# Performance work log

Measured on AMD Instinct MI355X. Metric: run time of the kernel, lower is better.

Reference implementation:

```python
import jax, jax.numpy as jnp
import numpy as np

TOP_K = 2
TEMP = 1.0  # router_temperature
B, L, D, F, DF, DR, DH, E = 32, 256, 256, 8, 64, 256, 512, 8
DIN = D + DF  # expert/router input: concat(hidden, feat_emb)


def setup_inputs() -> dict:
    key = jax.random.key(0)
    ks = jax.random.split(key, 12)
    gn = lambda k, shape, fan: jax.random.normal(k, shape, dtype=jnp.float32) * (fan ** -0.5)
    return {
        "hidden": jax.random.normal(ks[0], (B, L, D), dtype=jnp.float32),
        "feat": jax.random.uniform(ks[1], (B, L, F), dtype=jnp.float32),
        "W_feat": gn(ks[2], (F, DF), F),
        "b_feat": jnp.zeros((DF,), jnp.float32),
        "Wr1": gn(ks[3], (DIN, DR), DIN),
        "br1": jnp.zeros((DR,), jnp.float32),
        "Wr2": gn(ks[4], (DR, E), DR),
        "br2": jnp.zeros((E,), jnp.float32),
        "We1": gn(ks[5], (E, DIN, DH), DIN),
        "be1": jnp.zeros((E, DH), jnp.float32),
        "We2": gn(ks[6], (E, DH, D), DH),
        "be2": jnp.zeros((E, D), jnp.float32),
    }


def reference(hidden, feat, W_feat, b_feat, Wr1, br1, Wr2, br2, We1, be1, We2, be2):
    # feature embedding
    feat_emb = feat @ W_feat + b_feat                       # [B,L,DF]
    x = jnp.concatenate([hidden, feat_emb], axis=-1)        # [B,L,DIN]

    # token-level learned router with temperature + top-k gating
    hr = jax.nn.gelu(x @ Wr1 + br1)                         # [B,L,DR]
    gate_logits = (hr @ Wr2 + br2) / TEMP                   # [B,L,E]
    topv, topi = jax.lax.top_k(gate_logits, TOP_K)          # [B,L,K]
    w = jax.nn.softmax(topv, axis=-1)                       # renormalized over top-k
    gate_weights = (jax.nn.one_hot(topi, E, dtype=w.dtype) * w[..., None]).sum(-2)  # [B,L,E]

    # experts: per-expert 2-layer MLP (dense compute, sparse combine via gates)
    he = jax.nn.gelu(jnp.einsum('bli,eih->bleh', x, We1) + be1)   # [B,L,E,DH]
    eo = jnp.einsum('bleh,eho->bleo', he, We2) + be2              # [B,L,E,D]
    stage_delta = jnp.einsum('ble,bleo->blo', gate_weights, eo)   # next_hidden - hidden

    return stage_delta, gate_weights, gate_logits
```

## Files before the change

### kernel.cpp

```cpp
#include <hip/hip_runtime.h>
#include <hip/hip_bf16.h>

#define N_TOK   8192
#define DMODEL  256
#define NFEAT   8
#define DFEAT   64
#define DIN     320
#define DRTR    256
#define NE      8
#define DH      512
#define TE      32
#define RTB     32
#define FIXCAP  128
#define FIXTHR  2e-3f

#define OUT_GATEW  (N_TOK*DMODEL)
#define OUT_LOGITS (N_TOK*DMODEL + N_TOK*NE)

typedef short v8s __attribute__((ext_vector_type(8)));
typedef float v4f __attribute__((ext_vector_type(4)));

__device__ __forceinline__ unsigned short f2bf(float f){
  unsigned u = __float_as_uint(f);
  return (unsigned short)((u + 0x7FFFu + ((u>>16)&1u)) >> 16);
}
__device__ __forceinline__ float bf2f(unsigned short h){
  return __uint_as_float(((unsigned)h)<<16);
}
__device__ __forceinline__ float gelu_tanh(float v){
  float u = 0.7978845608028654f * (v + 0.044715f * v * v * v);
  float a = fabsf(u);
  float e = __expf(-2.0f * a);
  float t = (1.0f - e) / (1.0f + e);
  t = copysignf(t, u);
  return 0.5f * v * (1.0f + t);
}

__global__ void k_init(int* __restrict__ cnts, int* __restrict__ nfix){
  if (threadIdx.x < NE) cnts[threadIdx.x] = 0;
  if (threadIdx.x == NE) *nfix = 0;
}

__global__ __launch_bounds__(256) void k_prep1(const float* __restrict__ W,
                                               unsigned short* __restrict__ dh,
                                               unsigned short* __restrict__ dl){
  int gid = blockIdx.x*256 + threadIdx.x;
  int l = gid & 63; int w = gid >> 6;
  int nt = w & 31; w >>= 5; int kstep = w % 10; int e = w / 10;
  int n = nt*16 + (l&15);
  int kb = kstep*32 + ((l>>4)<<3);
  const float* src = W + ((size_t)e*DIN + kb)*DH + n;
  unsigned short hs[8], ls[8];
  #pragma unroll
  for (int i=0;i<8;i++){
    float v = src[(size_t)i*DH];
    unsigned short h = f2bf(v);
    hs[i] = h; ls[i] = f2bf(v - bf2f(h));
  }
  size_t off = (size_t)gid*8;
  *(v8s*)(dh+off) = *(v8s*)hs;
  *(v8s*)(dl+off) = *(v8s*)ls;
}

__global__ __launch_bounds__(256) void k_prep2(const float* __restrict__ W,
                                               unsigned short* __restrict__ dh,
                                               unsigned short* __restrict__ dl){
  int gid = blockIdx.x*256 + threadIdx.x;
  int l = gid & 63; int w = gid >> 6;
  int nt = w & 15; w >>= 4; int kstep = w & 15; int e = w >> 4;
  int n = nt*16 + (l&15);
  int kb = kstep*32 + ((l>>4)<<3);
  const float* src = W + ((size_t)e*DH + kb)*DMODEL + n;
  unsigned short hs[8], ls[8];
  #pragma unroll
  for (int i=0;i<8;i++){
    float v = src[(size_t)i*DMODEL];
    unsigned short h = f2bf(v);
    hs[i] = h; ls[i] = f2bf(v - bf2f(h));
  }
  size_t off = (size_t)gid*8;
  *(v8s*)(dh+off) = *(v8s*)hs;
  *(v8s*)(dl+off) = *(v8s*)ls;
}

__global__ __launch_bounds__(256) void k_prepr(const float* __restrict__ W,
                                               unsigned short* __restrict__ dh,
                                               unsigned short* __restrict__ dl){
  int gid = blockIdx.x*256 + threadIdx.x;
  if (gid >= 10240) return;
  int l = gid & 63; int w = gid >> 6;
  int nt = w & 15; int kstep = w >> 4;
  int n = nt*16 + (l&15);
  int kb = kstep*32 + ((l>>4)<<3);
  const float* src = W + (size_t)kb*DRTR + n;
  unsigned short hs[8], ls[8];
  #pragma unroll
  for (int i=0;i<8;i++){
    float v = src[(size_t)i*DRTR];
    unsigned short h = f2bf(v);
    hs[i] = h; ls[i] = f2bf(v - bf2f(h));
  }
  size_t off = (size_t)gid*8;
  *(v8s*)(dh+off) = *(v8s*)hs;
  *(v8s*)(dl+off) = *(v8s*)ls;
}

#define MM6(c0,c1,ah0,ah1,al0,al1,bh,bl) do{ \
  c0 = __builtin_amdgcn_mfma_f32_16x16x32_bf16(ah0, bh, c0, 0,0,0); \
  c1 = __builtin_amdgcn_mfma_f32_16x16x32_bf16(ah1, bh, c1, 0,0,0); \
  c0 = __builtin_amdgcn_mfma_f32_16x16x32_bf16(al0, bh, c0, 0,0,0); \
  c1 = __builtin_amdgcn_mfma_f32_16x16x32_bf16(al1, bh, c1, 0,0,0); \
  c0 = __builtin_amdgcn_mfma_f32_16x16x32_bf16(ah0, bl, c0, 0,0,0); \
  c1 = __builtin_amdgcn_mfma_f32_16x16x32_bf16(ah1, bl, c1, 0,0,0); }while(0)

#define XLOFF  10496
#define HELOFF 16640

__global__ __launch_bounds__(512) void k_rmfma(
    const float* __restrict__ hidden, const float* __restrict__ feat,
    const float* __restrict__ Wf, const float* __restrict__ bfe,
    const unsigned short* __restrict__ Wr1h, const unsigned short* __restrict__ Wr1l,
    const float* __restrict__ br1,
    const float* __restrict__ Wr2, const float* __restrict__ br2,
    float* __restrict__ out,
    int* __restrict__ cnts, unsigned* __restrict__ lists, float* __restrict__ topw,
    int* __restrict__ nfix, int* __restrict__ fixlist)
{
  __shared__ unsigned short sm[21248];
  __shared__ float part_lds[512];
  __shared__ float lg_lds[RTB*NE];
  float* hrf = (float*)sm;
  const int tid = threadIdx.x;
  const int t0 = blockIdx.x * RTB;

  {
    float4 z = make_float4(0.f,0.f,0.f,0.f);
    float4* dst = ((float4*)out) + (size_t)blockIdx.x*2048 + tid;
    #pragma unroll
    for (int r=0;r<4;r++) dst[r*512] = z;
  }
  #pragma unroll
  for (int r=0;r<4;r++){
    int idx = r*512 + tid; int t = idx >> 6, lane = idx & 63;
    float4 h4 = ((const float4*)(hidden + (size_t)(t0+t)*DMODEL))[lane];
    unsigned short h0=f2bf(h4.x),h1=f2bf(h4.y),h2=f2bf(h4.z),h3=f2bf(h4.w);
    unsigned short l0=f2bf(h4.x-bf2f(h0)),l1=f2bf(h4.y-bf2f(h1)),
                   l2=f2bf(h4.z-bf2f(h2)),l3=f2bf(h4.w-bf2f(h3));
    uint2 hp, lp;
    hp.x=(unsigned)h0|((unsigned)h1<<16); hp.y=(unsigned)h2|((unsigned)h3<<16);
    lp.x=(unsigned)l0|((unsigned)l1<<16); lp.y=(unsigned)l2|((unsigned)l3<<16);
    *(uint2*)&sm[t*328 + lane*4]         = hp;
    *(uint2*)&sm[XLOFF + t*328 + lane*4] = lp;
  }
  #pragma unroll
  for (int r=0;r<4;r++){
    int idx = r*512 + tid; int t = idx >> 6, j = idx & 63;
    float acc = bfe[j];
    #pragma unroll
    for (int f=0; f<NFEAT; f++) acc += feat[(size_t)(t0+t)*NFEAT + f] * Wf[f*DFEAT + j];
    unsigned short h = f2bf(acc);
    sm[t*328 + DMODEL + j]         = h;
    sm[XLOFF + t*328 + DMODEL + j] = f2bf(acc - bf2f(h));
  }
  __syncthreads();

  const int wv = tid >> 6;
  const int l  = tid & 63;
  const int lg = l >> 4;
  const int lr = l & 15;

  v4f acc[2][2];
  {
    v4f z = {0.f,0.f,0.f,0.f};
    acc[0][0]=z; acc[0][1]=z; acc[1][0]=z; acc[1][1]=z;
    v8s bh_a[2], bl_a[2], bh_b[2], bl_b[2];
    auto ldBr = [&](int ks, v8s (&bh)[2], v8s (&bl)[2]){
      #pragma unroll
      for (int j=0;j<2;++j){
        size_t boff = ((size_t)(ks*16 + wv*2 + j)*64 + l)*8;
        bh[j] = *(const v8s*)(Wr1h + boff);
        bl[j] = *(const v8s*)(Wr1l + boff);
      }
    };
    ldBr(0, bh_a, bl_a);
    for (int ks=0; ks<10; ks+=2){
      v8s ah0 = *(const v8s*)&sm[( 0+lr)*328 + ks*32 + lg*8];
      v8s ah1 = *(const v8s*)&sm[(16+lr)*328 + ks*32 + lg*8];
      v8s al0 = *(const v8s*)&sm[XLOFF + ( 0+lr)*328 + ks*32 + lg*8];
      v8s al1 = *(const v8s*)&sm[XLOFF + (16+lr)*328 + ks*32 + lg*8];
      ldBr(ks+1, bh_b, bl_b);
      #pragma unroll
      for (int j=0;j<2;++j) MM6(acc[0][j],acc[1][j], ah0,ah1,al0,al1, bh_a[j],bl_a[j]);
      v8s ch0 = *(const v8s*)&sm[( 0+lr)*328 + (ks+1)*32 + lg*8];
      v8s ch1 = *(const v8s*)&sm[(16+lr)*328 + (ks+1)*32 + lg*8];
      v8s cl0 = *(const v8s*)&sm[XLOFF + ( 0+lr)*328 + (ks+1)*32 + lg*8];
      v8s cl1 = *(const v8s*)&sm[XLOFF + (16+lr)*328 + (ks+1)*32 + lg*8];
      if (ks+2<10) ldBr(ks+2, bh_a, bl_a);
      #pragma unroll
      for (int j=0;j<2;++j) MM6(acc[0][j],acc[1][j], ch0,ch1,cl0,cl1, bh_b[j],bl_b[j]);
    }
  }
  __syncthreads();
  #pragma unroll
  for (int j=0;j<2;++j){
    int col = (wv*2+j)*16 + lr;
    float b1 = br1[col];
    #pragma unroll
    for (int m=0;m<2;m++)
      #pragma unroll
      for (int r=0;r<4;r++){
        int row = m*16 + lg*4 + r;
        hrf[row*264 + col] = gelu_tanh(acc[m][j][r] + b1);
      }
  }
  __syncthreads();
  {
    int q = tid >> 8, rr = tid & 255, t = rr >> 3, e = rr & 7;
    float a0=0.f,a1=0.f,a2=0.f,a3=0.f;
    #pragma unroll 4
    for (int k4=0;k4<32;k4++){
      float4 h4 = ((const float4*)hrf)[t*66 + q*32 + k4];
      int row = q*128 + k4*4;
      a0 += h4.x * Wr2[(row+0)*NE + e];
      a1 += h4.y * Wr2[(row+1)*NE + e];
      a2 += h4.z * Wr2[(row+2)*NE + e];
      a3 += h4.w * Wr2[(row+3)*NE + e];
    }
    part_lds[tid] = (a0+a1)+(a2+a3);
  }
  __syncthreads();
  if (tid < RTB*NE){
    int t = tid >> 3, e = tid & 7;
    float lgv = br2[e] + part_lds[tid] + part_lds[tid+256];
    out[OUT_LOGITS + (size_t)(t0+t)*NE + e] = lgv;
    lg_lds[t*NE + e] = lgv;
  }
  __syncthreads();
  if (tid < RTB){
    int t = tid, tok = t0 + t;
    float v1=-3.4e38f, v2=-3.4e38f, v3=-3.4e38f; int i1=-1, i2=-1;
    #pragma unroll
    for (int e=0;e<NE;e++){
      float v = lg_lds[t*NE+e];
      if (v > v1){ v3=v2; v2=v1; i2=i1; v1=v; i1=e; }
      else if (v > v2){ v3=v2; v2=v; i2=e; }
      else if (v > v3){ v3=v; }
    }
    bool defer = false;
    if (v2 - v3 < FIXTHR){
      int fi = atomicAdd(nfix, 1);
      if (fi < FIXCAP){ fixlist[fi] = tok; defer = true; }
    }
    if (!defer){
      float d   = expf(v2 - v1);
      float inv = 1.0f/(1.0f + d);
      float w1 = inv, w2 = d*inv;
      #pragma unroll
      for (int e=0;e<NE;e++){
        float gv = (e==i1) ? w1 : ((e==i2) ? w2 : 0.f);
        out[OUT_GATEW + (size_t)tok*NE + e] = gv;
      }
      int p1 = atomicAdd(&cnts[i1], 1);
      lists[i1*N_TOK + p1] = (unsigned)(tok<<1);
      int p2 = atomicAdd(&cnts[i2], 1);
      lists[i2*N_TOK + p2] = (unsigned)((tok<<1) | 1);
      topw[tok*2]   = w1;
      topw[tok*2+1] = w2;
    }
  }
}

__global__ __launch_bounds__(256) void k_fix(
    const float* __restrict__ hidden, const float* __restrict__ feat,
    const float* __restrict__ Wf, const float* __restrict__ bfe,
    const float* __restrict__ Wr1, const float* __restrict__ br1,
    const float* __restrict__ Wr2, const float* __restrict__ br2,
    float* __restrict__ out, const int* __restrict__ nfix, const int* __restrict__ fixlist)
{
  int nf = *nfix; if (nf > FIXCAP) nf = FIXCAP;
  if ((int)blockIdx.x >= nf) return;
  const int tok = fixlist[blockIdx.x];
  const int tid = threadIdx.x;
  __shared__ float xf[DIN];
  __shared__ float hr[DRTR];
  if (tid < DMODEL) xf[tid] = hidden[(size_t)tok*DMODEL + tid];
  if (tid < DFEAT){
    float acc = bfe[tid];
    #pragma unroll
    for (int f=0; f<NFEAT; f++) acc += feat[(size_t)tok*NFEAT + f] * Wf[f*DFEAT + tid];
    xf[DMODEL + tid] = acc;
  }
  __syncthreads();
  {
    float acc = br1[tid];
    for (int i=0;i<DIN;i++) acc += xf[i] * Wr1[(size_t)i*DRTR + tid];
    hr[tid] = gelu_tanh(acc);
  }
  __syncthreads();
  if (tid < NE){
    float acc = br2[tid];
    for (int i=0;i<DRTR;i++) acc += hr[i] * Wr2[i*NE + tid];
    out[OUT_LOGITS + (size_t)tok*NE + tid] = acc;
  }
}

__global__ void k_gatefix(float* __restrict__ out,
                          int* __restrict__ cnts, unsigned* __restrict__ lists,
                          float* __restrict__ topw,
                          const int* __restrict__ nfix, const int* __restrict__ fixlist)
{
  int nf = *nfix; if (nf > FIXCAP) nf = FIXCAP;
  int i = threadIdx.x;
  if (i >= nf) return;
  int tok = fixlist[i];
  float v1=-3.4e38f, v2=-3.4e38f; int i1=-1, i2=-1;
  #pragma unroll
  for (int e=0;e<NE;e++){
    float v = out[OUT_LOGITS + (size_t)tok*NE + e];
    if (v > v1){ v2=v1; i2=i1; v1=v; i1=e; }
    else if (v > v2){ v2=v; i2=e; }
  }
  float d   = expf(v2 - v1);
  float inv = 1.0f/(1.0f + d);
  float w1 = inv, w2 = d*inv;
  #pragma unroll
  for (int e=0;e<NE;e++){
    float gv = (e==i1) ? w1 : ((e==i2) ? w2 : 0.f);
    out[OUT_GATEW + (size_t)tok*NE + e] = gv;
  }
  int p1 = atomicAdd(&cnts[i1], 1);
  lists[i1*N_TOK + p1] = (unsigned)(tok<<1);
  int p2 = atomicAdd(&cnts[i2], 1);
  lists[i2*N_TOK + p2] = (unsigned)((tok<<1) | 1);
  topw[tok*2]   = w1;
  topw[tok*2+1] = w2;
}

__global__ __launch_bounds__(512) void k_expert(
    const float* __restrict__ hidden, const float* __restrict__ feat,
    const float* __restrict__ Wf, const float* __restrict__ bfe,
    const int* __restrict__ cnts, const unsigned* __restrict__ lists,
    const float* __restrict__ topw,
    const unsigned short* __restrict__ W1h, const unsigned short* __restrict__ W1l,
    const unsigned short* __restrict__ W2h, const unsigned short* __restrict__ W2l,
    const float* __restrict__ be1, const float* __restrict__ be2,
    float* __restrict__ out)
{
  __shared__ unsigned short sm[33280];
  __shared__ int   tok_lds[TE];
  __shared__ float w_lds[TE];

  const int e    = blockIdx.x & 7;
  const int tile = blockIdx.x >> 3;
  const int cnt  = cnts[e];
  const int start = tile * TE;
  if (start >= cnt) return;
  const int ntk = min(TE, cnt - start);
  const int tid = threadIdx.x;

  if (tid < TE){
    if (tid < ntk){
      unsigned ent = lists[e*N_TOK + start + tid];
      int tok = (int)(ent >> 1);
      tok_lds[tid] = tok;
      w_lds[tid]   = topw[tok*2 + (ent & 1)];
    } else { tok_lds[tid] = -1; w_lds[tid] = 0.f; }
  }
  __syncthreads();
  #pragma unroll
  for (int r=0;r<4;r++){
    int idx = r*512 + tid; int t = idx >> 6, lane = idx & 63;
    int tok = tok_lds[t];
    float4 h4 = make_float4(0.f,0.f,0.f,0.f);
    if (tok >= 0) h4 = ((const float4*)(hidden + (size_t)tok*DMODEL))[lane];
    unsigned short h0=f2bf(h4.x),h1=f2bf(h4.y),h2=f2bf(h4.z),h3=f2bf(h4.w);
    unsigned short l0=f2bf(h4.x-bf2f(h0)),l1=f2bf(h4.y-bf2f(h1)),
                   l2=f2bf(h4.z-bf2f(h2)),l3=f2bf(h4.w-bf2f(h3));
    uint2 hp, lp;
    hp.x=(unsigned)h0|((unsigned)h1<<16); hp.y=(unsigned)h2|((unsigned)h3<<16);
    lp.x=(unsigned)l0|((unsigned)l1<<16); lp.y=(unsigned)l2|((unsigned)l3<<16);
    *(uint2*)&sm[t*328 + lane*4]         = hp;
    *(uint2*)&sm[XLOFF + t*328 + lane*4] = lp;
  }
  #pragma unroll
  for (int r=0;r<4;r++){
    int idx = r*512 + tid; int t = idx >> 6, j = idx & 63;
    int tok = tok_lds[t];
    float acc = 0.f;
    if (tok >= 0){
      acc = bfe[j];
      #pragma unroll
      for (int f=0; f<NFEAT; f++) acc += feat[(size_t)tok*NFEAT + f] * Wf[f*DFEAT + j];
    }
    unsigned short h = f2bf(acc);
    sm[t*328 + DMODEL + j]         = h;
    sm[XLOFF + t*328 + DMODEL + j] = f2bf(acc - bf2f(h));
  }
  __syncthreads();

  const int wv = tid >> 6;
  const int l  = tid & 63;
  const int lg = l >> 4;
  const int lr = l & 15;

  v4f acc1[2][4];
  {
    v4f z = {0.f,0.f,0.f,0.f};
    #pragma unroll
    for (int m=0;m<2;m++)
      #pragma unroll
      for (int j=0;j<4;j++) acc1[m][j] = z;
    const unsigned short* p1h = W1h + (size_t)e*163840;
    const unsigned short* p1l = W1l + (size_t)e*163840;
    auto ldB1 = [&](int ks, int jh, v8s (&bh)[2], v8s (&bl)[2]){
      #pragma unroll
      for (int j=0;j<2;++j){
        size_t boff = ((size_t)(ks*32 + wv*4 + jh*2 + j)*64 + l)*8;
        bh[j] = *(const v8s*)(p1h + boff);
        bl[j] = *(const v8s*)(p1l + boff);
      }
    };
    v8s bh_a[2], bl_a[2], bh_b[2], bl_b[2];
    ldB1(0,0,bh_a,bl_a);
    for (int ks=0; ks<10; ++ks){
      v8s ah0 = *(const v8s*)&sm[( 0+lr)*328 + ks*32 + lg*8];
      v8s ah1 = *(const v8s*)&sm[(16+lr)*328 + ks*32 + lg*8];
      v8s al0 = *(const v8s*)&sm[XLOFF + ( 0+lr)*328 + ks*32 + lg*8];
      v8s al1 = *(const v8s*)&sm[XLOFF + (16+lr)*328 + ks*32 + lg*8];
      ldB1(ks,1,bh_b,bl_b);
      #pragma unroll
      for (int j=0;j<2;++j) MM6(acc1[0][j],acc1[1][j], ah0,ah1,al0,al1, bh_a[j],bl_a[j]);
      if (ks<9) ldB1(ks+1,0,bh_a,bl_a);
      #pragma unroll
      for (int j=0;j<2;++j) MM6(acc1[0][2+j],acc1[1][2+j], ah0,ah1,al0,al1, bh_b[j],bl_b[j]);
    }
  }
  __syncthreads();
  #pragma unroll
  for (int j=0;j<4;++j){
    int col = (wv*4+j)*16 + lr;
    float b1 = be1[e*DH + col];
    #pragma unroll
    for (int m=0;m<2;m++)
      #pragma unroll
      for (int r=0;r<4;r++){
        float v = gelu_tanh(acc1[m][j][r] + b1);
        int row = m*16 + lg*4 + r;
        unsigned short h = f2bf(v);
        sm[row*520 + col]          = h;
        sm[HELOFF + row*520 + col] = f2bf(v - bf2f(h));
      }
  }
  __syncthreads();
  v4f acc2[2][2];
  {
    v4f z = {0.f,0.f,0.f,0.f};
    acc2[0][0]=z; acc2[0][1]=z; acc2[1][0]=z; acc2[1][1]=z;
    const unsigned short* p2h = W2h + (size_t)e*131072;
    const unsigned short* p2l = W2l + (size_t)e*131072;
    auto ldB2 = [&](int ks, v8s (&bh)[2], v8s (&bl)[2]){
      #pragma unroll
      for (int j=0;j<2;++j){
        size_t boff = ((size_t)(ks*16 + wv*2 + j)*64 + l)*8;
        bh[j] = *(const v8s*)(p2h + boff);
        bl[j] = *(const v8s*)(p2l + boff);
      }
    };
    v8s bh_a[2], bl_a[2], bh_b[2], bl_b[2];
    ldB2(0,bh_a,bl_a);
    for (int ks=0; ks<16; ks+=2){
      v8s ah0 = *(const v8s*)&sm[( 0+lr)*520 + ks*32 + lg*8];
      v8s ah1 = *(const v8s*)&sm[(16+lr)*520 + ks*32 + lg*8];
      v8s al0 = *(const v8s*)&sm[HELOFF + ( 0+lr)*520 + ks*32 + lg*8];
      v8s al1 = *(const v8s*)&sm[HELOFF + (16+lr)*520 + ks*32 + lg*8];
      ldB2(ks+1, bh_b, bl_b);
      #pragma unroll
      for (int j=0;j<2;++j) MM6(acc2[0][j],acc2[1][j], ah0,ah1,al0,al1, bh_a[j],bl_a[j]);
      v8s ch0 = *(const v8s*)&sm[( 0+lr)*520 + (ks+1)*32 + lg*8];
      v8s ch1 = *(const v8s*)&sm[(16+lr)*520 + (ks+1)*32 + lg*8];
      v8s cl0 = *(const v8s*)&sm[HELOFF + ( 0+lr)*520 + (ks+1)*32 + lg*8];
      v8s cl1 = *(const v8s*)&sm[HELOFF + (16+lr)*520 + (ks+1)*32 + lg*8];
      if (ks+2<16) ldB2(ks+2, bh_a, bl_a);
      #pragma unroll
      for (int j=0;j<2;++j) MM6(acc2[0][j],acc2[1][j], ch0,ch1,cl0,cl1, bh_b[j],bl_b[j]);
    }
  }
  #pragma unroll
  for (int j=0;j<2;++j){
    int col = (wv*2+j)*16 + lr;
    float b2 = be2[e*DMODEL + col];
    #pragma unroll
    for (int m=0;m<2;m++)
      #pragma unroll
      for (int r=0;r<4;r++){
        int row = m*16 + lg*4 + r;
        if (row < ntk){
          float w = w_lds[row];
          atomicAdd(out + (size_t)tok_lds[row]*DMODEL + col,
                    w*(acc2[m][j][r] + b2));
        }
      }
  }
}

extern "C" void kernel_launch(void* const* d_in, const int* in_sizes, int n_in,
                              void* d_out, int out_size, void* d_ws, size_t ws_size,
                              hipStream_t stream)
{
  (void)in_sizes; (void)n_in; (void)out_size; (void)ws_size;
  const float* hidden = (const float*)d_in[0];
  const float* feat   = (const float*)d_in[1];
  const float* Wf     = (const float*)d_in[2];
  const float* bfe    = (const float*)d_in[3];
  const float* Wr1    = (const float*)d_in[4];
  const float* br1    = (const float*)d_in[5];
  const float* Wr2    = (const float*)d_in[6];
  const float* br2    = (const float*)d_in[7];
  const float* We1    = (const float*)d_in[8];
  const float* be1    = (const float*)d_in[9];
  const float* We2    = (const float*)d_in[10];
  const float* be2    = (const float*)d_in[11];
  float* out = (float*)d_out;

  char* ws = (char*)d_ws;
  int*      cnts    = (int*)ws;
  int*      nfix    = (int*)(ws + 64);
  int*      fixlist = (int*)(ws + 128);
  unsigned* lists   = (unsigned*)(ws + 1024);
  float*    topw    = (float*)(ws + 263168);
  unsigned short* W1h  = (unsigned short*)(ws + 328704);
  unsigned short* W1l  = (unsigned short*)(ws + 2950144);
  unsigned short* W2h  = (unsigned short*)(ws + 5571584);
  unsigned short* W2l  = (unsigned short*)(ws + 7668736);
  unsigned short* Wr1h = (unsigned short*)(ws + 9765888);
  unsigned short* Wr1l = (unsigned short*)(ws + 9929728);

  hipLaunchKernelGGL(k_init, dim3(1), dim3(64), 0, stream, cnts, nfix);
  hipLaunchKernelGGL(k_prep1, dim3(640), dim3(256), 0, stream, We1, W1h, W1l);
  hipLaunchKernelGGL(k_prep2, dim3(512), dim3(256), 0, stream, We2, W2h, W2l);
  hipLaunchKernelGGL(k_prepr, dim3(40),  dim3(256), 0, stream, Wr1, Wr1h, Wr1l);
  hipLaunchKernelGGL(k_rmfma, dim3(N_TOK/RTB), dim3(512), 0, stream,
                     hidden, feat, Wf, bfe, Wr1h, Wr1l, br1, Wr2, br2,
                     out, cnts, lists, topw, nfix, fixlist);
  hipLaunchKernelGGL(k_fix, dim3(FIXCAP), dim3(256), 0, stream,
                     hidden, feat, Wf, bfe, Wr1, br1, Wr2, br2, out, nfix, fixlist);
  hipLaunchKernelGGL(k_gatefix, dim3(1), dim3(FIXCAP), 0, stream,
                     out, cnts, lists, topw, nfix, fixlist);
  hipLaunchKernelGGL(k_expert, dim3((N_TOK/TE)*NE), dim3(512), 0, stream,
                     hidden, feat, Wf, bfe, cnts, lists, topw,
                     W1h, W1l, W2h, W2l, be1, be2, out);
}
```

Baseline: 293.8 us.

## Double expert token tile to 64 with 1024-thread blocks; merge prep kernels

The expert kernel now processes 64 routed tokens per block with 16 waves instead of 32 tokens with 8 waves. Each wave owns fewer output columns but more row tiles, so every bf16 hi/lo expert weight fragment loaded from global memory is reused across twice as many tokens. The first weight fragments are prefetched before the token gather to hide load latency. Separately, the three weight-split prep kernels and the counter-init kernel are merged into one launch to cut launch overhead. The cost is about 133KB of LDS per block, which limits occupancy to one block per CU, and more padded work on the last partial tile of each expert.

```diff
diff --git a/kernel.cpp b/kernel.cpp
--- a/kernel.cpp
+++ b/kernel.cpp
@@ -9,7 +9,7 @@
 #define DRTR    256
 #define NE      8
 #define DH      512
-#define TE      32
+#define TE      64
 #define RTB     32
 #define FIXCAP  128
 #define FIXTHR  2e-3f
@@ -36,73 +36,71 @@
   return 0.5f * v * (1.0f + t);
 }
 
-__global__ void k_init(int* __restrict__ cnts, int* __restrict__ nfix){
-  if (threadIdx.x < NE) cnts[threadIdx.x] = 0;
-  if (threadIdx.x == NE) *nfix = 0;
-}
-
-__global__ __launch_bounds__(256) void k_prep1(const float* __restrict__ W,
-                                               unsigned short* __restrict__ dh,
-                                               unsigned short* __restrict__ dl){
-  int gid = blockIdx.x*256 + threadIdx.x;
-  int l = gid & 63; int w = gid >> 6;
-  int nt = w & 31; w >>= 5; int kstep = w % 10; int e = w / 10;
-  int n = nt*16 + (l&15);
-  int kb = kstep*32 + ((l>>4)<<3);
-  const float* src = W + ((size_t)e*DIN + kb)*DH + n;
-  unsigned short hs[8], ls[8];
-  #pragma unroll
-  for (int i=0;i<8;i++){
-    float v = src[(size_t)i*DH];
-    unsigned short h = f2bf(v);
-    hs[i] = h; ls[i] = f2bf(v - bf2f(h));
-  }
-  size_t off = (size_t)gid*8;
-  *(v8s*)(dh+off) = *(v8s*)hs;
-  *(v8s*)(dl+off) = *(v8s*)ls;
-}
-
-__global__ __launch_bounds__(256) void k_prep2(const float* __restrict__ W,
-                                               unsigned short* __restrict__ dh,
-                                               unsigned short* __restrict__ dl){
-  int gid = blockIdx.x*256 + threadIdx.x;
-  int l = gid & 63; int w = gid >> 6;
-  int nt = w & 15; w >>= 4; int kstep = w & 15; int e = w >> 4;
-  int n = nt*16 + (l&15);
-  int kb = kstep*32 + ((l>>4)<<3);
-  const float* src = W + ((size_t)e*DH + kb)*DMODEL + n;
-  unsigned short hs[8], ls[8];
-  #pragma unroll
-  for (int i=0;i<8;i++){
-    float v = src[(size_t)i*DMODEL];
-    unsigned short h = f2bf(v);
-    hs[i] = h; ls[i] = f2bf(v - bf2f(h));
-  }
-  size_t off = (size_t)gid*8;
-  *(v8s*)(dh+off) = *(v8s*)hs;
-  *(v8s*)(dl+off) = *(v8s*)ls;
-}
-
-__global__ __launch_bounds__(256) void k_prepr(const float* __restrict__ W,
-                                               unsigned short* __restrict__ dh,
-                                               unsigned short* __restrict__ dl){
-  int gid = blockIdx.x*256 + threadIdx.x;
-  if (gid >= 10240) return;
-  int l = gid & 63; int w = gid >> 6;
-  int nt = w & 15; int kstep = w >> 4;
-  int n = nt*16 + (l&15);
-  int kb = kstep*32 + ((l>>4)<<3);
-  const float* src = W + (size_t)kb*DRTR + n;
-  unsigned short hs[8], ls[8];
-  #pragma unroll
-  for (int i=0;i<8;i++){
-    float v = src[(size_t)i*DRTR];
-    unsigned short h = f2bf(v);
-    hs[i] = h; ls[i] = f2bf(v - bf2f(h));
-  }
-  size_t off = (size_t)gid*8;
-  *(v8s*)(dh+off) = *(v8s*)hs;
-  *(v8s*)(dl+off) = *(v8s*)ls;
+__global__ __launch_bounds__(256) void k_prep(
+    const float* __restrict__ We1, const float* __restrict__ We2,
+    const float* __restrict__ Wr1,
+    unsigned short* __restrict__ W1h, unsigned short* __restrict__ W1l,
+    unsigned short* __restrict__ W2h, unsigned short* __restrict__ W2l,
+    unsigned short* __restrict__ Wr1h, unsigned short* __restrict__ Wr1l,
+    int* __restrict__ cnts, int* __restrict__ nfix)
+{
+  const int b = blockIdx.x;
+  const int tid = threadIdx.x;
+  if (b < 640){
+    int gid = b*256 + tid;
+    int l = gid & 63; int w = gid >> 6;
+    int nt = w & 31; w >>= 5; int kstep = w % 10; int e = w / 10;
+    int n = nt*16 + (l&15);
+    int kb = kstep*32 + ((l>>4)<<3);
+    const float* src = We1 + ((size_t)e*DIN + kb)*DH + n;
+    unsigned short hs[8], ls[8];
+    #pragma unroll
+    for (int i=0;i<8;i++){
+      float v = src[(size_t)i*DH];
+      unsigned short h = f2bf(v);
+      hs[i] = h; ls[i] = f2bf(v - bf2f(h));
+    }
+    size_t off = (size_t)gid*8;
+    *(v8s*)(W1h+off) = *(v8s*)hs;
+    *(v8s*)(W1l+off) = *(v8s*)ls;
+  } else if (b < 1152){
+    int gid = (b-640)*256 + tid;
+    int l = gid & 63; int w = gid >> 6;
+    int nt = w & 15; w >>= 4; int kstep = w & 15; int e = w >> 4;
+    int n = nt*16 + (l&15);
+    int kb = kstep*32 + ((l>>4)<<3);
+    const float* src = We2 + ((size_t)e*DH + kb)*DMODEL + n;
+    unsigned short hs[8], ls[8];
+    #pragma unroll
+    for (int i=0;i<8;i++){
+      float v = src[(size_t)i*DMODEL];
+      unsigned short h = f2bf(v);
+      hs[i] = h; ls[i] = f2bf(v - bf2f(h));
+    }
+    size_t off = (size_t)gid*8;
+    *(v8s*)(W2h+off) = *(v8s*)hs;
+    *(v8s*)(W2l+off) = *(v8s*)ls;
+  } else if (b < 1192){
+    int gid = (b-1152)*256 + tid;
+    int l = gid & 63; int w = gid >> 6;
+    int nt = w & 15; int kstep = w >> 4;
+    int n = nt*16 + (l&15);
+    int kb = kstep*32 + ((l>>4)<<3);
+    const float* src = Wr1 + (size_t)kb*DRTR + n;
+    unsigned short hs[8], ls[8];
+    #pragma unroll
+    for (int i=0;i<8;i++){
+      float v = src[(size_t)i*DRTR];
+      unsigned short h = f2bf(v);
+      hs[i] = h; ls[i] = f2bf(v - bf2f(h));
+    }
+    size_t off = (size_t)gid*8;
+    *(v8s*)(Wr1h+off) = *(v8s*)hs;
+    *(v8s*)(Wr1l+off) = *(v8s*)ls;
+  } else {
+    if (tid < NE) cnts[tid] = 0;
+    if (tid == NE) *nfix = 0;
+  }
 }
 
 #define MM6(c0,c1,ah0,ah1,al0,al1,bh,bl) do{ \
@@ -114,7 +112,6 @@
   c1 = __builtin_amdgcn_mfma_f32_16x16x32_bf16(ah1, bl, c1, 0,0,0); }while(0)
 
 #define XLOFF  10496
-#define HELOFF 16640
 
 __global__ __launch_bounds__(512) void k_rmfma(
     const float* __restrict__ hidden, const float* __restrict__ feat,
@@ -336,7 +333,9 @@
   topw[tok*2+1] = w2;
 }
 
-__global__ __launch_bounds__(512) void k_expert(
+#define XL2   20992
+#define HEL2  33280
+__global__ __launch_bounds__(1024, 4) void k_expert(
     const float* __restrict__ hidden, const float* __restrict__ feat,
     const float* __restrict__ Wf, const float* __restrict__ bfe,
     const int* __restrict__ cnts, const unsigned* __restrict__ lists,
@@ -346,7 +345,7 @@
     const float* __restrict__ be1, const float* __restrict__ be2,
     float* __restrict__ out)
 {
-  __shared__ unsigned short sm[33280];
+  __shared__ unsigned short sm[66560];
   __shared__ int   tok_lds[TE];
   __shared__ float w_lds[TE];
 
@@ -357,6 +356,21 @@
   if (start >= cnt) return;
   const int ntk = min(TE, cnt - start);
   const int tid = threadIdx.x;
+  const int wv = tid >> 6;
+  const int l  = tid & 63;
+  const int lg = l >> 4;
+  const int lr = l & 15;
+
+  const unsigned short* p1h = W1h + (size_t)e*163840;
+  const unsigned short* p1l = W1l + (size_t)e*163840;
+
+  v8s bhA[2], blA[2], bhB[2], blB[2];
+  #pragma unroll
+  for (int j=0;j<2;++j){
+    size_t boff = ((size_t)(wv*2 + j)*64 + l)*8;
+    bhA[j] = *(const v8s*)(p1h + boff);
+    blA[j] = *(const v8s*)(p1l + boff);
+  }
 
   if (tid < TE){
     if (tid < ntk){
@@ -369,7 +383,7 @@
   __syncthreads();
   #pragma unroll
   for (int r=0;r<4;r++){
-    int idx = r*512 + tid; int t = idx >> 6, lane = idx & 63;
+    int idx = r*1024 + tid; int t = idx >> 6, lane = idx & 63;
     int tok = tok_lds[t];
     float4 h4 = make_float4(0.f,0.f,0.f,0.f);
     if (tok >= 0) h4 = ((const float4*)(hidden + (size_t)tok*DMODEL))[lane];
@@ -379,12 +393,12 @@
     uint2 hp, lp;
     hp.x=(unsigned)h0|((unsigned)h1<<16); hp.y=(unsigned)h2|((unsigned)h3<<16);
     lp.x=(unsigned)l0|((unsigned)l1<<16); lp.y=(unsigned)l2|((unsigned)l3<<16);
-    *(uint2*)&sm[t*328 + lane*4]         = hp;
-    *(uint2*)&sm[XLOFF + t*328 + lane*4] = lp;
+    *(uint2*)&sm[t*328 + lane*4]       = hp;
+    *(uint2*)&sm[XL2 + t*328 + lane*4] = lp;
   }
   #pragma unroll
   for (int r=0;r<4;r++){
-    int idx = r*512 + tid; int t = idx >> 6, j = idx & 63;
+    int idx = r*1024 + tid; int t = idx >> 6, j = idx & 63;
     int tok = tok_lds[t];
     float acc = 0.f;
     if (tok >= 0){
@@ -393,111 +407,140 @@
       for (int f=0; f<NFEAT; f++) acc += feat[(size_t)tok*NFEAT + f] * Wf[f*DFEAT + j];
     }
     unsigned short h = f2bf(acc);
-    sm[t*328 + DMODEL + j]         = h;
-    sm[XLOFF + t*328 + DMODEL + j] = f2bf(acc - bf2f(h));
-  }
-  __syncthreads();
-
-  const int wv = tid >> 6;
-  const int l  = tid & 63;
-  const int lg = l >> 4;
-  const int lr = l & 15;
-
-  v4f acc1[2][4];
+    sm[t*328 + DMODEL + j]       = h;
+    sm[XL2 + t*328 + DMODEL + j] = f2bf(acc - bf2f(h));
+  }
+  __syncthreads();
+
+  v4f acc1[4][2];
   {
     v4f z = {0.f,0.f,0.f,0.f};
     #pragma unroll
-    for (int m=0;m<2;m++)
-      #pragma unroll
-      for (int j=0;j<4;j++) acc1[m][j] = z;
-    const unsigned short* p1h = W1h + (size_t)e*163840;
-    const unsigned short* p1l = W1l + (size_t)e*163840;
-    auto ldB1 = [&](int ks, int jh, v8s (&bh)[2], v8s (&bl)[2]){
+    for (int m=0;m<4;m++){ acc1[m][0]=z; acc1[m][1]=z; }
+    for (int ks=0; ks<10; ks+=2){
+      v8s ah[4], al[4];
+      #pragma unroll
+      for (int m=0;m<4;m++){
+        ah[m] = *(const v8s*)&sm[(m*16+lr)*328 + ks*32 + lg*8];
+        al[m] = *(const v8s*)&sm[XL2 + (m*16+lr)*328 + ks*32 + lg*8];
+      }
       #pragma unroll
       for (int j=0;j<2;++j){
-        size_t boff = ((size_t)(ks*32 + wv*4 + jh*2 + j)*64 + l)*8;
-        bh[j] = *(const v8s*)(p1h + boff);
-        bl[j] = *(const v8s*)(p1l + boff);
-      }
-    };
-    v8s bh_a[2], bl_a[2], bh_b[2], bl_b[2];
-    ldB1(0,0,bh_a,bl_a);
-    for (int ks=0; ks<10; ++ks){
-      v8s ah0 = *(const v8s*)&sm[( 0+lr)*328 + ks*32 + lg*8];
-      v8s ah1 = *(const v8s*)&sm[(16+lr)*328 + ks*32 + lg*8];
-      v8s al0 = *(const v8s*)&sm[XLOFF + ( 0+lr)*328 + ks*32 + lg*8];
-      v8s al1 = *(const v8s*)&sm[XLOFF + (16+lr)*328 + ks*32 + lg*8];
-      ldB1(ks,1,bh_b,bl_b);
-      #pragma unroll
-      for (int j=0;j<2;++j) MM6(acc1[0][j],acc1[1][j], ah0,ah1,al0,al1, bh_a[j],bl_a[j]);
-      if (ks<9) ldB1(ks+1,0,bh_a,bl_a);
-      #pragma unroll
-      for (int j=0;j<2;++j) MM6(acc1[0][2+j],acc1[1][2+j], ah0,ah1,al0,al1, bh_b[j],bl_b[j]);
-    }
-  }
-  __syncthreads();
-  #pragma unroll
-  for (int j=0;j<4;++j){
-    int col = (wv*4+j)*16 + lr;
+        size_t boff = ((size_t)((ks+1)*32 + wv*2 + j)*64 + l)*8;
+        bhB[j] = *(const v8s*)(p1h + boff);
+        blB[j] = *(const v8s*)(p1l + boff);
+      }
+      #pragma unroll
+      for (int j=0;j<2;++j){
+        #pragma unroll
+        for (int m=0;m<4;m++) acc1[m][j] = __builtin_amdgcn_mfma_f32_16x16x32_bf16(ah[m], bhA[j], acc1[m][j], 0,0,0);
+        #pragma unroll
+        for (int m=0;m<4;m++) acc1[m][j] = __builtin_amdgcn_mfma_f32_16x16x32_bf16(al[m], bhA[j], acc1[m][j], 0,0,0);
+        #pragma unroll
+        for (int m=0;m<4;m++) acc1[m][j] = __builtin_amdgcn_mfma_f32_16x16x32_bf16(ah[m], blA[j], acc1[m][j], 0,0,0);
+      }
+      #pragma unroll
+      for (int m=0;m<4;m++){
+        ah[m] = *(const v8s*)&sm[(m*16+lr)*328 + (ks+1)*32 + lg*8];
+        al[m] = *(const v8s*)&sm[XL2 + (m*16+lr)*328 + (ks+1)*32 + lg*8];
+      }
+      if (ks+2<10){
+        #pragma unroll
+        for (int j=0;j<2;++j){
+          size_t boff = ((size_t)((ks+2)*32 + wv*2 + j)*64 + l)*8;
+          bhA[j] = *(const v8s*)(p1h + boff);
+          blA[j] = *(const v8s*)(p1l + boff);
+        }
+      }
+      #pragma unroll
+      for (int j=0;j<2;++j){
+        #pragma unroll
+        for (int m=0;m<4;m++) acc1[m][j] = __builtin_amdgcn_mfma_f32_16x16x32_bf16(ah[m], bhB[j], acc1[m][j], 0,0,0);
+        #pragma unroll
+        for (int m=0;m<4;m++) acc1[m][j] = __builtin_amdgcn_mfma_f32_16x16x32_bf16(al[m], bhB[j], acc1[m][j], 0,0,0);
+        #pragma unroll
+        for (int m=0;m<4;m++) acc1[m][j] = __builtin_amdgcn_mfma_f32_16x16x32_bf16(ah[m], blB[j], acc1[m][j], 0,0,0);
+      }
+    }
+  }
+  const unsigned short* p2h = W2h + (size_t)e*131072;
+  const unsigned short* p2l = W2l + (size_t)e*131072;
+  v8s c2hA, c2lA, c2hB, c2lB;
+  {
+    size_t boff = ((size_t)wv*64 + l)*8;
+    c2hA = *(const v8s*)(p2h + boff);
+    c2lA = *(const v8s*)(p2l + boff);
+  }
+  __syncthreads();
+  #pragma unroll
+  for (int j=0;j<2;++j){
+    int col = (wv*2+j)*16 + lr;
     float b1 = be1[e*DH + col];
     #pragma unroll
-    for (int m=0;m<2;m++)
+    for (int m=0;m<4;m++)
       #pragma unroll
       for (int r=0;r<4;r++){
         float v = gelu_tanh(acc1[m][j][r] + b1);
         int row = m*16 + lg*4 + r;
         unsigned short h = f2bf(v);
-        sm[row*520 + col]          = h;
-        sm[HELOFF + row*520 + col] = f2bf(v - bf2f(h));
-      }
-  }
-  __syncthreads();
-  v4f acc2[2][2];
+        sm[row*520 + col]        = h;
+        sm[HEL2 + row*520 + col] = f2bf(v - bf2f(h));
+      }
+  }
+  __syncthreads();
+  v4f acc2[4];
   {
     v4f z = {0.f,0.f,0.f,0.f};
-    acc2[0][0]=z; acc2[0][1]=z; acc2[1][0]=z; acc2[1][1]=z;
-    const unsigned short* p2h = W2h + (size_t)e*131072;
-    const unsigned short* p2l = W2l + (size_t)e*131072;
-    auto ldB2 = [&](int ks, v8s (&bh)[2], v8s (&bl)[2]){
-      #pragma unroll
-      for (int j=0;j<2;++j){
-        size_t boff = ((size_t)(ks*16 + wv*2 + j)*64 + l)*8;
-        bh[j] = *(const v8s*)(p2h + boff);
-        bl[j] = *(const v8s*)(p2l + boff);
-      }
-    };
-    v8s bh_a[2], bl_a[2], bh_b[2], bl_b[2];
-    ldB2(0,bh_a,bl_a);
+    #pragma unroll
+    for (int m=0;m<4;m++) acc2[m] = z;
     for (int ks=0; ks<16; ks+=2){
-      v8s ah0 = *(const v8s*)&sm[( 0+lr)*520 + ks*32 + lg*8];
-      v8s ah1 = *(const v8s*)&sm[(16+lr)*520 + ks*32 + lg*8];
-      v8s al0 = *(const v8s*)&sm[HELOFF + ( 0+lr)*520 + ks*32 + lg*8];
-      v8s al1 = *(const v8s*)&sm[HELOFF + (16+lr)*520 + ks*32 + lg*8];
-      ldB2(ks+1, bh_b, bl_b);
-      #pragma unroll
-      for (int j=0;j<2;++j) MM6(acc2[0][j],acc2[1][j], ah0,ah1,al0,al1, bh_a[j],bl_a[j]);
-      v8s ch0 = *(const v8s*)&sm[( 0+lr)*520 + (ks+1)*32 + lg*8];
-      v8s ch1 = *(const v8s*)&sm[(16+lr)*520 + (ks+1)*32 + lg*8];
-      v8s cl0 = *(const v8s*)&sm[HELOFF + ( 0+lr)*520 + (ks+1)*32 + lg*8];
-      v8s cl1 = *(const v8s*)&sm[HELOFF + (16+lr)*520 + (ks+1)*32 + lg*8];
-      if (ks+2<16) ldB2(ks+2, bh_a, bl_a);
-      #pragma unroll
-      for (int j=0;j<2;++j) MM6(acc2[0][j],acc2[1][j], ch0,ch1,cl0,cl1, bh_b[j],bl_b[j]);
-    }
-  }
-  #pragma unroll
-  for (int j=0;j<2;++j){
-    int col = (wv*2+j)*16 + lr;
+      v8s ah[4], al[4];
+      #pragma unroll
+      for (int m=0;m<4;m++){
+        ah[m] = *(const v8s*)&sm[(m*16+lr)*520 + ks*32 + lg*8];
+        al[m] = *(const v8s*)&sm[HEL2 + (m*16+lr)*520 + ks*32 + lg*8];
+      }
+      {
+        size_t boff = ((size_t)((ks+1)*16 + wv)*64 + l)*8;
+        c2hB = *(const v8s*)(p2h + boff);
+        c2lB = *(const v8s*)(p2l + boff);
+      }
+      #pragma unroll
+      for (int m=0;m<4;m++) acc2[m] = __builtin_amdgcn_mfma_f32_16x16x32_bf16(ah[m], c2hA, acc2[m], 0,0,0);
+      #pragma unroll
+      for (int m=0;m<4;m++) acc2[m] = __builtin_amdgcn_mfma_f32_16x16x32_bf16(al[m], c2hA, acc2[m], 0,0,0);
+      #pragma unroll
+      for (int m=0;m<4;m++) acc2[m] = __builtin_amdgcn_mfma_f32_16x16x32_bf16(ah[m], c2lA, acc2[m], 0,0,0);
+      #pragma unroll
+      for (int m=0;m<4;m++){
+        ah[m] = *(const v8s*)&sm[(m*16+lr)*520 + (ks+1)*32 + lg*8];
+        al[m] = *(const v8s*)&sm[HEL2 + (m*16+lr)*520 + (ks+1)*32 + lg*8];
+      }
+      if (ks+2<16){
+        size_t boff = ((size_t)((ks+2)*16 + wv)*64 + l)*8;
+        c2hA = *(const v8s*)(p2h + boff);
+        c2lA = *(const v8s*)(p2l + boff);
+      }
+      #pragma unroll
+      for (int m=0;m<4;m++) acc2[m] = __builtin_amdgcn_mfma_f32_16x16x32_bf16(ah[m], c2hB, acc2[m], 0,0,0);
+      #pragma unroll
+      for (int m=0;m<4;m++) acc2[m] = __builtin_amdgcn_mfma_f32_16x16x32_bf16(al[m], c2hB, acc2[m], 0,0,0);
+      #pragma unroll
+      for (int m=0;m<4;m++) acc2[m] = __builtin_amdgcn_mfma_f32_16x16x32_bf16(ah[m], c2lB, acc2[m], 0,0,0);
+    }
+  }
+  {
+    int col = wv*16 + lr;
     float b2 = be2[e*DMODEL + col];
     #pragma unroll
-    for (int m=0;m<2;m++)
+    for (int m=0;m<4;m++)
       #pragma unroll
       for (int r=0;r<4;r++){
         int row = m*16 + lg*4 + r;
         if (row < ntk){
           float w = w_lds[row];
           atomicAdd(out + (size_t)tok_lds[row]*DMODEL + col,
-                    w*(acc2[m][j][r] + b2));
+                    w*(acc2[m][r] + b2));
         }
       }
   }
@@ -535,10 +578,8 @@
   unsigned short* Wr1h = (unsigned short*)(ws + 9765888);
   unsigned short* Wr1l = (unsigned short*)(ws + 9929728);
 
-  hipLaunchKernelGGL(k_init, dim3(1), dim3(64), 0, stream, cnts, nfix);
-  hipLaunchKernelGGL(k_prep1, dim3(640), dim3(256), 0, stream, We1, W1h, W1l);
-  hipLaunchKernelGGL(k_prep2, dim3(512), dim3(256), 0, stream, We2, W2h, W2l);
-  hipLaunchKernelGGL(k_prepr, dim3(40),  dim3(256), 0, stream, Wr1, Wr1h, Wr1l);
+  hipLaunchKernelGGL(k_prep, dim3(1193), dim3(256), 0, stream,
+                     We1, We2, Wr1, W1h, W1l, W2h, W2l, Wr1h, Wr1l, cnts, nfix);
   hipLaunchKernelGGL(k_rmfma, dim3(N_TOK/RTB), dim3(512), 0, stream,
                      hidden, feat, Wf, bfe, Wr1h, Wr1l, br1, Wr2, br2,
                      out, cnts, lists, topw, nfix, fixlist);
@@ -546,7 +587,7 @@
                      hidden, feat, Wf, bfe, Wr1, br1, Wr2, br2, out, nfix, fixlist);
   hipLaunchKernelGGL(k_gatefix, dim3(1), dim3(FIXCAP), 0, stream,
                      out, cnts, lists, topw, nfix, fixlist);
-  hipLaunchKernelGGL(k_expert, dim3((N_TOK/TE)*NE), dim3(512), 0, stream,
+  hipLaunchKernelGGL(k_expert, dim3((N_TOK/TE)*NE*2), dim3(1024), 0, stream,
                      hidden, feat, Wf, bfe, cnts, lists, topw,
                      W1h, W1l, W2h, W2l, be1, be2, out);
 }
```

Result: slower. 303.5 us (+3.3%).
